# Optimization experiments

Hardware: AMD Instinct MI355X
Metric: run time of the kernel (lower is better)

Reference implementation:

```python
import jax, jax.numpy as jnp
import numpy as np

N_NODES = 50000


def gcn_conv(x, edge_index, W, b):
    """PyG GCNConv: add self-loops, sym-normalize, out = A_hat @ (x W) + b."""
    src, dst = edge_index[0], edge_index[1]
    n = x.shape[0]
    h = x @ W  # [N, out]
    # degree with self-loops (all edge weights = 1)
    deg = jax.ops.segment_sum(jnp.ones_like(dst, dtype=x.dtype), dst, num_segments=n) + 1.0
    dinv = jax.lax.rsqrt(deg)  # deg >= 1 so safe
    norm = dinv[src] * dinv[dst]  # [E]
    msgs = h[src] * norm[:, None]  # gather + scale
    agg = jax.ops.segment_sum(msgs, dst, num_segments=n)  # scatter-add
    agg = agg + h * (dinv * dinv)[:, None]  # self-loop term: norm_ii = dinv_i^2
    return agg + b


def setup_inputs() -> dict:
    key = jax.random.key(0)
    k_x, k_e, k_w1, k_w2 = jax.random.split(key, 4)
    in_ch, hid, out_ch = 256, 128, 128
    x = jax.random.normal(k_x, (N_NODES, in_ch), dtype=jnp.float32)
    edge_index = jax.random.randint(k_e, (2, 1_600_000), 0, N_NODES, dtype=jnp.int32)
    # Glorot-style init like PyG GCNConv
    W1 = jax.random.normal(k_w1, (in_ch, hid), dtype=jnp.float32) * (1.0 / np.sqrt(in_ch))
    b1 = jnp.zeros((hid,), dtype=jnp.float32)
    W2 = jax.random.normal(k_w2, (hid, out_ch), dtype=jnp.float32) * (1.0 / np.sqrt(hid))
    b2 = jnp.zeros((out_ch,), dtype=jnp.float32)
    return {"x": x, "edge_index": edge_index, "W1": W1, "b1": b1, "W2": W2, "b2": b2}


def reference(x, edge_index, W1, b1, W2, b2):
    # layer 1: GCNConv -> ReLU (dropout is identity in eval mode)
    h = jax.nn.relu(gcn_conv(x, edge_index, W1, b1))
    # layer 2: GCNConv -> ReLU
    out = jax.nn.relu(gcn_conv(h, edge_index, W2, b2))
    return out
```

## Files before the change

### kernel.cpp

```cpp
#include <hip/hip_runtime.h>
#include <cstdint>
#include <cstddef>


#define ELL_STRIDE 64
#define BCAP 8192
#define OVF_CAP 1024
#define PART_T 2048

typedef __attribute__((ext_vector_type(8))) short bf16x8;
typedef __attribute__((ext_vector_type(4))) float floatx4;

__device__ __forceinline__ unsigned short f2bf(float f) {
  unsigned int u = __float_as_uint(f);
  unsigned int r = (u + 0x7fffu + ((u >> 16) & 1u)) >> 16;
  return (unsigned short)r;
}
__device__ __forceinline__ float2 bfpair(unsigned int p) {
  float2 r;
  r.x = __uint_as_float(p << 16);
  r.y = __uint_as_float(p & 0xffff0000u);
  return r;
}

__global__ __launch_bounds__(256) void k_cvt_w(const float* __restrict__ W1,
                                               const float* __restrict__ W2,
                                               unsigned short* __restrict__ WT1,
                                               unsigned short* __restrict__ WT2,
                                               int* __restrict__ cursor,
                                               int* __restrict__ ovf_cnt,
                                               unsigned short* __restrict__ hb,
                                               int N, int NB) {
  int i = blockIdx.x * 256 + threadIdx.x;
  if (i < NB) cursor[i] = 0;
  if (i == NB) *ovf_cnt = 0;
  if (i < 128) {
    int chunk = i >> 6, j = i & 63;
    hb[(size_t)chunk * (N + 1) * 64 + (size_t)N * 64 + j] = 0;
  }
  if (i < 128 * 256) {
    int n = i >> 8, k = i & 255;
    WT1[i] = f2bf(W1[k * 128 + n]);
  } else if (i < 128 * 256 + 128 * 128) {
    int j = i - 128 * 256;
    int n = j >> 7, k = j & 127;
    WT2[j] = f2bf(W2[k * 128 + n]);
  }
}

__global__ __launch_bounds__(256) void k_part(const int* __restrict__ src,
                                              const int* __restrict__ dst,
                                              int* __restrict__ cursor,
                                              unsigned int* __restrict__ part,
                                              int* __restrict__ ovf_cnt,
                                              int* __restrict__ ovf,
                                              int E, int NB) {
  __shared__ unsigned int stage1[PART_T];
  __shared__ unsigned int stage2[PART_T];
  __shared__ int hist[512];
  __shared__ int base_g[512];
  __shared__ int base_l[512];
  __shared__ int cl[512];
  __shared__ int sc[256];
  const int tid = threadIdx.x;
  const int e0 = blockIdx.x * PART_T;
  int valid = E - e0; if (valid > PART_T) valid = PART_T;

  hist[tid] = 0; hist[tid + 256] = 0;
  cl[tid] = 0; cl[tid + 256] = 0;
  __syncthreads();
  for (int i = tid; i < valid; i += 256) {
    int e = e0 + i;
    unsigned int v = (unsigned int)(src[e] & 0xffff) | ((unsigned int)dst[e] << 16);
    stage1[i] = v;
    atomicAdd(&hist[(v >> 16) >> 7], 1);
  }
  __syncthreads();
  for (int b = tid; b < NB; b += 256) base_g[b] = atomicAdd(&cursor[b], hist[b]);
  int h0 = hist[2 * tid], h1 = hist[2 * tid + 1];
  int pv = h0 + h1;
  sc[tid] = pv;
  __syncthreads();
  #pragma unroll
  for (int off = 1; off < 256; off <<= 1) {
    int t = (tid >= off) ? sc[tid - off] : 0;
    __syncthreads();
    sc[tid] += t;
    __syncthreads();
  }
  int excl = sc[tid] - pv;
  base_l[2 * tid] = excl;
  base_l[2 * tid + 1] = excl + h0;
  __syncthreads();
  for (int i = tid; i < valid; i += 256) {
    unsigned int v = stage1[i];
    int b = (v >> 16) >> 7;
    int pos = base_l[b] + atomicAdd(&cl[b], 1);
    stage2[pos] = v;
  }
  __syncthreads();
  for (int i = tid; i < valid; i += 256) {
    unsigned int v = stage2[i];
    int b = (v >> 16) >> 7;
    int g = base_g[b] + (i - base_l[b]);
    if (g < BCAP) {
      part[(size_t)b * BCAP + g] = v;
    } else {
      int p = atomicAdd(ovf_cnt, 1);
      if (p < OVF_CAP) { ovf[2 * p] = (int)(v & 0xffffu); ovf[2 * p + 1] = (int)(v >> 16); }
    }
  }
}

__global__ __launch_bounds__(256) void k_fill2(const unsigned int* __restrict__ part,
                                               const int* __restrict__ cursor,
                                               unsigned short* __restrict__ col,
                                               int* __restrict__ cnt,
                                               float* __restrict__ dinv,
                                               int* __restrict__ ovf_cnt,
                                               int* __restrict__ ovf, int N) {
  __shared__ unsigned short slab[128 * ELL_STRIDE];
  __shared__ int cl[128];
  const int tid = threadIdx.x;
  const int b = blockIdx.x;
  if (tid < 128) cl[tid] = 0;
  {
    unsigned int dpk = ((unsigned int)N << 16) | (unsigned int)N;
    unsigned int* s32 = (unsigned int*)slab;
    #pragma unroll
    for (int i = 0; i < (128 * ELL_STRIDE / 2) / 256; ++i)
      s32[i * 256 + tid] = dpk;
  }
  __syncthreads();
  int count = cursor[b]; if (count > BCAP) count = BCAP;
  const unsigned int* p = part + (size_t)b * BCAP;
  for (int i = tid; i < count; i += 256) {
    unsigned int v = p[i];
    int row = (v >> 16) & 127;
    int k = atomicAdd(&cl[row], 1);
    if (k < ELL_STRIDE) {
      slab[row * ELL_STRIDE + k] = (unsigned short)(v & 0xffffu);
    } else {
      int q = atomicAdd(ovf_cnt, 1);
      if (q < OVF_CAP) { ovf[2 * q] = (int)(v & 0xffffu); ovf[2 * q + 1] = (int)(v >> 16); }
    }
  }
  __syncthreads();
  uint4* d4 = (uint4*)(col + (size_t)b * 128 * ELL_STRIDE);
  const uint4* s4 = (const uint4*)slab;
  #pragma unroll
  for (int i = 0; i < (128 * ELL_STRIDE * 2) / (16 * 256); ++i)
    d4[i * 256 + tid] = s4[i * 256 + tid];
  if (tid < 128) {
    int node = b * 128 + tid;
    if (node < N) {
      int c = cl[tid];
      cnt[node] = c;
      dinv[node] = rsqrtf((float)c + 1.0f);
    }
  }
}

template <int K, bool AF32>
__global__ __launch_bounds__(512) void k_gemm_mfma(const void* __restrict__ Xv,
                                                   const unsigned short* __restrict__ WT,
                                                   const float* __restrict__ dinv,
                                                   unsigned short* __restrict__ hb,
                                                   int M) {
  constexpr int KP = K + 8;
  __shared__ unsigned short Bs[128 * KP];
  const int tid = threadIdx.x;
  const int wave = tid >> 6, lane = tid & 63;
  const int q = lane >> 4, m = lane & 15;
  const int row0 = blockIdx.x * 128 + wave * 16;
  const bool active = row0 < M;
  const int arow = row0 + m;

  for (int c = tid; c < 128 * (K / 8); c += 512) {
    int r = c / (K / 8), ko = (c % (K / 8)) * 8;
    *(uint4*)(Bs + r * KP + ko) = *(const uint4*)(WT + (size_t)r * K + ko);
  }

  bf16x8 af[K / 32];
  if (active) {
    #pragma unroll
    for (int ks = 0; ks < K / 32; ++ks) {
      const int k0 = ks * 32 + q * 8;
      if (AF32) {
        const float* X = (const float*)Xv;
        float4 a0 = *(const float4*)(X + (size_t)arow * K + k0);
        float4 a1 = *(const float4*)(X + (size_t)arow * K + k0 + 4);
        af[ks] = (bf16x8){(short)f2bf(a0.x), (short)f2bf(a0.y),
                          (short)f2bf(a0.z), (short)f2bf(a0.w),
                          (short)f2bf(a1.x), (short)f2bf(a1.y),
                          (short)f2bf(a1.z), (short)f2bf(a1.w)};
      } else {
        af[ks] = *(const bf16x8*)((const unsigned short*)Xv +
                                  (size_t)arow * K + k0);
      }
    }
  }
  __syncthreads();
  if (!active) return;

  floatx4 acc[8];
  #pragma unroll
  for (int nt = 0; nt < 8; ++nt) acc[nt] = (floatx4){0.f, 0.f, 0.f, 0.f};
  #pragma unroll
  for (int ks = 0; ks < K / 32; ++ks) {
    const int k0 = ks * 32 + q * 8;
    #pragma unroll
    for (int nt = 0; nt < 8; ++nt) {
      bf16x8 bf = *(const bf16x8*)(Bs + (nt * 16 + m) * KP + k0);
      acc[nt] = __builtin_amdgcn_mfma_f32_16x16x32_bf16(af[ks], bf, acc[nt], 0, 0, 0);
    }
  }
  #pragma unroll
  for (int r = 0; r < 4; ++r) {
    int grow = row0 + q * 4 + r;
    float di = dinv[grow];
    #pragma unroll
    for (int nt = 0; nt < 8; ++nt)
      hb[(size_t)(nt >> 2) * (M + 1) * 64 + (size_t)grow * 64 +
         (nt & 3) * 16 + m] = f2bf(acc[nt][r] * di);
  }
}

template <bool BF16OUT>
__global__ __launch_bounds__(256) void k_agg(const uint4* __restrict__ hb4,
                                             const int* __restrict__ cnt,
                                             const unsigned short* __restrict__ col,
                                             const float* __restrict__ dinv,
                                             const int* __restrict__ ovf_cnt,
                                             const int* __restrict__ ovf,
                                             const float* __restrict__ bias,
                                             void* __restrict__ outv, int n) {
  __shared__ unsigned short cols[32][72];
  const int tid = threadIdx.x;
  const int chunk = blockIdx.x & 1;
  const int nd0 = (blockIdx.x >> 1) * 32;
  {
    unsigned int dpk = ((unsigned int)n << 16) | (unsigned int)n;
    int node = tid >> 3, off = (tid & 7) * 8;
    uint4 v0 = make_uint4(dpk, dpk, dpk, dpk);
    if (nd0 + node < n)
      v0 = *(const uint4*)(col + (size_t)(nd0 + node) * ELL_STRIDE + off);
    *(uint4*)&cols[node][off] = v0;
  }
  __syncthreads();
  const int wave = tid >> 6, lane = tid & 63;
  const int nodeL = wave * 8 + (lane >> 3);
  const int q = lane & 7;
  const int d = nd0 + nodeL;
  const bool valid = d < n;
  const uint4* slab = hb4 + (size_t)chunk * (n + 1) * 8;
  const unsigned short* lc = cols[nodeL];

  float a0 = 0.f, a1 = 0.f, a2 = 0.f, a3 = 0.f;
  float a4 = 0.f, a5 = 0.f, a6 = 0.f, a7 = 0.f;
#define ADDP(P)                                                            \
  {                                                                        \
    float2 x0 = bfpair((P).x), x1 = bfpair((P).y);                         \
    float2 x2 = bfpair((P).z), x3 = bfpair((P).w);                         \
    a0 += x0.x; a1 += x0.y; a2 += x1.x; a3 += x1.y;                        \
    a4 += x2.x; a5 += x2.y; a6 += x3.x; a7 += x3.y;                        \
  }
  if (valid) {
    uint4 p = slab[(size_t)d * 8 + q];
    ADDP(p)
  }
  int m = valid ? cnt[d] : 0; if (m > ELL_STRIDE) m = ELL_STRIDE;
  int mmax = m;
  #pragma unroll
  for (int s = 8; s < 64; s <<= 1) {
    int o = __shfl_xor(mmax, s);
    mmax = o > mmax ? o : mmax;
  }
  for (int k = 0; k < mmax; k += 8) {
    ushort4 ca = *(const ushort4*)(lc + k);
    ushort4 cb = *(const ushort4*)(lc + k + 4);
    uint4 p0 = slab[(size_t)ca.x * 8 + q];
    uint4 p1 = slab[(size_t)ca.y * 8 + q];
    uint4 p2 = slab[(size_t)ca.z * 8 + q];
    uint4 p3 = slab[(size_t)ca.w * 8 + q];
    uint4 p4 = slab[(size_t)cb.x * 8 + q];
    uint4 p5 = slab[(size_t)cb.y * 8 + q];
    uint4 p6 = slab[(size_t)cb.z * 8 + q];
    uint4 p7 = slab[(size_t)cb.w * 8 + q];
    ADDP(p0) ADDP(p1) ADDP(p2) ADDP(p3)
    ADDP(p4) ADDP(p5) ADDP(p6) ADDP(p7)
  }
  if (valid) {
    int V = *ovf_cnt; if (V > OVF_CAP) V = OVF_CAP;
    for (int j = 0; j < V; ++j) {
      if (ovf[2 * j + 1] == d) {
        uint4 p = slab[(size_t)ovf[2 * j] * 8 + q];
        ADDP(p)
      }
    }
  }
#undef ADDP
  if (!valid) return;
  float di = dinv[d];
  float4 b0 = *(const float4*)(bias + chunk * 64 + q * 8);
  float4 b1 = *(const float4*)(bias + chunk * 64 + q * 8 + 4);
  float r0 = fmaxf(di * a0 + b0.x, 0.f);
  float r1 = fmaxf(di * a1 + b0.y, 0.f);
  float r2 = fmaxf(di * a2 + b0.z, 0.f);
  float r3 = fmaxf(di * a3 + b0.w, 0.f);
  float r4 = fmaxf(di * a4 + b1.x, 0.f);
  float r5 = fmaxf(di * a5 + b1.y, 0.f);
  float r6 = fmaxf(di * a6 + b1.z, 0.f);
  float r7 = fmaxf(di * a7 + b1.w, 0.f);
  if (BF16OUT) {
    uint4 pk;
    pk.x = (unsigned int)f2bf(r0) | ((unsigned int)f2bf(r1) << 16);
    pk.y = (unsigned int)f2bf(r2) | ((unsigned int)f2bf(r3) << 16);
    pk.z = (unsigned int)f2bf(r4) | ((unsigned int)f2bf(r5) << 16);
    pk.w = (unsigned int)f2bf(r6) | ((unsigned int)f2bf(r7) << 16);
    ((uint4*)outv)[(size_t)d * 16 + chunk * 8 + q] = pk;
  } else {
    float* o = (float*)outv + (size_t)d * 128 + chunk * 64 + q * 8;
    *(float4*)o = make_float4(r0, r1, r2, r3);
    *(float4*)(o + 4) = make_float4(r4, r5, r6, r7);
  }
}

extern "C" void kernel_launch(void* const* d_in, const int* in_sizes, int n_in,
                              void* d_out, int out_size, void* d_ws, size_t ws_size,
                              hipStream_t stream) {
  const float* x  = (const float*)d_in[0];
  const int*   ei = (const int*)d_in[1];
  const float* W1 = (const float*)d_in[2];
  const float* b1 = (const float*)d_in[3];
  const float* W2 = (const float*)d_in[4];
  const float* b2 = (const float*)d_in[5];
  float* out = (float*)d_out;

  const int IN_CH = 256;
  const int N = in_sizes[0] / IN_CH;
  const int E = in_sizes[1] / 2;
  const int NB = (N + 127) >> 7;

  const int* src = ei;
  const int* dst = ei + E;

  char* ws = (char*)d_ws;
  size_t off = 0;
  auto carve = [&](size_t bytes) {
    void* p = ws + off;
    off += (bytes + 255) & ~(size_t)255;
    return p;
  };
  int*            cursor  = (int*)carve((size_t)NB * 4);
  int*            ovf_cnt = (int*)carve(4);
  int*            ovf     = (int*)carve((size_t)OVF_CAP * 2 * 4);
  int*            cnt     = (int*)carve((size_t)N * 4);
  float*          dinv    = (float*)carve((size_t)N * 4);
  unsigned short* col     = (unsigned short*)carve((size_t)N * ELL_STRIDE * 2);
  unsigned short* hb      = (unsigned short*)carve((size_t)(N + 1) * 256);
  unsigned short* WT1     = (unsigned short*)carve(128 * 256 * 2);
  unsigned short* WT2     = (unsigned short*)carve(128 * 128 * 2);
  char*           unionp  = (char*)carve((size_t)NB * BCAP * 4);
  unsigned int*   part    = (unsigned int*)unionp;
  unsigned short* aggbuf  = (unsigned short*)unionp;

  k_cvt_w<<<(128 * 256 + 128 * 128 + 255) / 256, 256, 0, stream>>>(
      W1, W2, WT1, WT2, cursor, ovf_cnt, hb, N, NB);
  k_part <<<(E + PART_T - 1) / PART_T, 256, 0, stream>>>(src, dst, cursor, part,
                                                         ovf_cnt, ovf, E, NB);
  k_fill2<<<NB, 256, 0, stream>>>(part, cursor, col, cnt, dinv, ovf_cnt, ovf, N);

  int gblocks = (N + 127) / 128;
  int ablocks = 2 * ((N + 31) / 32);
  k_gemm_mfma<256, true ><<<gblocks, 512, 0, stream>>>(x, WT1, dinv, hb, N);
  k_agg<true ><<<ablocks, 256, 0, stream>>>((const uint4*)hb, cnt, col, dinv,
                                            ovf_cnt, ovf, b1, aggbuf, N);
  k_gemm_mfma<128, false><<<gblocks, 512, 0, stream>>>(aggbuf, WT2, dinv, hb, N);
  k_agg<false><<<ablocks, 256, 0, stream>>>((const uint4*)hb, cnt, col, dinv,
                                            ovf_cnt, ovf, b2, out, N);
}
```

Before: 227.4 us.

## Sort ELL neighbor lists approximately by source via hashed slot placement

Each node's neighbors are now placed into a 64-slot shared-memory row at a position proportional to the source index, using atomicCAS with linear probing, and then compacted. This yields neighbor lists roughly sorted by source node, which is meant to improve cache locality of the feature gathers in the aggregation kernels. In exchange the build kernel uses twice the shared memory (32-bit slots), does CAS probing, and runs a serial compaction pass per row.

```diff
diff --git a/kernel.cpp b/kernel.cpp
--- a/kernel.cpp
+++ b/kernel.cpp
@@ -7,6 +7,7 @@
 #define BCAP 8192
 #define OVF_CAP 1024
 #define PART_T 2048
+#define SENT 0xffffffffu
 
 typedef __attribute__((ext_vector_type(8))) short bf16x8;
 typedef __attribute__((ext_vector_type(4))) float floatx4;
@@ -119,38 +120,52 @@
                                                float* __restrict__ dinv,
                                                int* __restrict__ ovf_cnt,
                                                int* __restrict__ ovf, int N) {
-  __shared__ unsigned short slab[128 * ELL_STRIDE];
+  __shared__ unsigned int islab[128 * 65];
   __shared__ int cl[128];
   const int tid = threadIdx.x;
   const int b = blockIdx.x;
   if (tid < 128) cl[tid] = 0;
-  {
-    unsigned int dpk = ((unsigned int)N << 16) | (unsigned int)N;
-    unsigned int* s32 = (unsigned int*)slab;
-    #pragma unroll
-    for (int i = 0; i < (128 * ELL_STRIDE / 2) / 256; ++i)
-      s32[i * 256 + tid] = dpk;
-  }
-  __syncthreads();
+  for (int i = tid; i < 128 * 65; i += 256) islab[i] = SENT;
+  __syncthreads();
+  const unsigned int Msc = ((unsigned int)64 << 16) / (unsigned int)N;
   int count = cursor[b]; if (count > BCAP) count = BCAP;
   const unsigned int* p = part + (size_t)b * BCAP;
   for (int i = tid; i < count; i += 256) {
     unsigned int v = p[i];
     int row = (v >> 16) & 127;
+    unsigned int s16 = v & 0xffffu;
     int k = atomicAdd(&cl[row], 1);
     if (k < ELL_STRIDE) {
-      slab[row * ELL_STRIDE + k] = (unsigned short)(v & 0xffffu);
+      int s = (int)((s16 * Msc) >> 16);
+      unsigned int* base = islab + row * 65;
+      while (atomicCAS(&base[s], SENT, s16) != SENT) s = (s + 1) & 63;
     } else {
       int q = atomicAdd(ovf_cnt, 1);
-      if (q < OVF_CAP) { ovf[2 * q] = (int)(v & 0xffffu); ovf[2 * q + 1] = (int)(v >> 16); }
-    }
+      if (q < OVF_CAP) { ovf[2 * q] = (int)s16; ovf[2 * q + 1] = (int)(v >> 16); }
+    }
+  }
+  __syncthreads();
+  if (tid < 128) {
+    unsigned int* base = islab + tid * 65;
+    int w = 0;
+    for (int j = 0; j < 64; ++j) {
+      unsigned int v = base[j];
+      if (v != SENT) base[w++] = v;
+    }
+    for (int j = w; j < 64; ++j) base[j] = (unsigned int)N;
   }
   __syncthreads();
   uint4* d4 = (uint4*)(col + (size_t)b * 128 * ELL_STRIDE);
-  const uint4* s4 = (const uint4*)slab;
-  #pragma unroll
-  for (int i = 0; i < (128 * ELL_STRIDE * 2) / (16 * 256); ++i)
-    d4[i * 256 + tid] = s4[i * 256 + tid];
+  for (int idx = tid; idx < 128 * 8; idx += 256) {
+    int node = idx >> 3, grp = idx & 7;
+    const unsigned int* bp = islab + node * 65 + grp * 8;
+    uint4 o;
+    o.x = (bp[0] & 0xffffu) | (bp[1] << 16);
+    o.y = (bp[2] & 0xffffu) | (bp[3] << 16);
+    o.z = (bp[4] & 0xffffu) | (bp[5] << 16);
+    o.w = (bp[6] & 0xffffu) | (bp[7] << 16);
+    d4[idx] = o;
+  }
   if (tid < 128) {
     int node = b * 128 + tid;
     if (node < N) {
```

After: 236.7 us. 1.04x slower.
